# Kernel tuning notes

Measured on AMD Instinct MI355X. Metric: run time of the kernel, lower is better.

## Reference

```python
import jax, jax.numpy as jnp
import numpy as np

N_NODES = 50000
N_EDGES = 1600000
N_GRAPHS = 64
F_IN = 256
H = 1024
EPS = 1e-5


def setup_inputs() -> dict:
    key = jax.random.key(0)
    ks = jax.random.split(key, 6)
    x = jax.random.normal(ks[0], (N_NODES, F_IN), dtype=jnp.float32)
    edge_index = jax.random.randint(ks[1], (2, N_EDGES), 0, N_NODES, dtype=jnp.int32)
    batch = jnp.sort(jax.random.randint(ks[2], (N_NODES,), 0, N_GRAPHS, dtype=jnp.int32))
    # Glorot-ish init for GCN weights
    W0 = jax.random.normal(ks[3], (F_IN, H), dtype=jnp.float32) * (1.0 / np.sqrt(F_IN))
    b0 = jnp.zeros((H,), dtype=jnp.float32)
    Ws = jax.random.normal(ks[4], (3, H, H), dtype=jnp.float32) * (1.0 / np.sqrt(H))
    bs = jnp.zeros((3, H), dtype=jnp.float32)
    gammas = jnp.ones((4, H), dtype=jnp.float32)
    betas = jnp.zeros((4, H), dtype=jnp.float32)
    return {"x": x, "edge_index": edge_index, "batch": batch,
            "W0": W0, "b0": b0, "Ws": Ws, "bs": bs,
            "gammas": gammas, "betas": betas}


def _gcn_norm(edge_index, n_nodes):
    # Add self-loops (PyG GCNConv default), compute symmetric normalization.
    loops = jnp.arange(n_nodes, dtype=edge_index.dtype)
    row = jnp.concatenate([edge_index[0], loops])  # sources
    col = jnp.concatenate([edge_index[1], loops])  # targets (aggregation index)
    ones = jnp.ones(row.shape[0], dtype=jnp.float32)
    deg = jax.ops.segment_sum(ones, col, num_segments=n_nodes)
    dinv = jnp.where(deg > 0, jax.lax.rsqrt(deg), 0.0)
    norm = dinv[row] * dinv[col]  # [E + N]
    return row, col, norm


def _layer(h, W, b, gamma, beta, row, col, norm):
    ht = h @ W                                           # [N, H] GEMM
    msg = ht[row] * norm[:, None]                        # gather + scale
    agg = jax.ops.segment_sum(msg, col, num_segments=N_NODES) + b
    mu = jnp.mean(agg, axis=-1, keepdims=True)
    var = jnp.mean(jnp.square(agg - mu), axis=-1, keepdims=True)
    hn = (agg - mu) * jax.lax.rsqrt(var + EPS) * gamma + beta
    return jax.nn.relu(hn)


def reference(x, edge_index, batch, W0, b0, Ws, bs, gammas, betas):
    row, col, norm = _gcn_norm(edge_index, N_NODES)
    h = _layer(x, W0, b0, gammas[0], betas[0], row, col, norm)
    for i in range(3):
        h = _layer(h, Ws[i], bs[i], gammas[i + 1], betas[i + 1], row, col, norm)
    # scatter_mean over batch (graph-level pooling)
    sums = jax.ops.segment_sum(h, batch, num_segments=N_GRAPHS)
    cnt = jax.ops.segment_sum(jnp.ones((N_NODES,), jnp.float32), batch, num_segments=N_GRAPHS)
    return sums / jnp.maximum(cnt, 1.0)[:, None]
```

## Files before the change

kernel.cpp:

```cpp
#include <hip/hip_runtime.h>
#include <hip/hip_bf16.h>
#include <stdint.h>

#define NN 50000
#define NE 1600000
#define NG 64
#define FIN 256
#define HD 1024
#define EPSV 1e-5f

typedef __bf16 bf16;
typedef float f32x4 __attribute__((ext_vector_type(4)));
typedef int i32x4 __attribute__((ext_vector_type(4)));

typedef const __attribute__((address_space(1))) void* gptr_as1;
typedef __attribute__((address_space(3))) void* lptr_as3;

__device__ __forceinline__ void load_g2l_16(const void* g, const void* l) {
  __builtin_amdgcn_global_load_lds((gptr_as1)(uintptr_t)g,
                                   (lptr_as3)(uint32_t)(uintptr_t)l, 16, 0, 0);
}

__global__ void hist_kernel(const int* __restrict__ col, int* __restrict__ cnt, int E) {
  int e = blockIdx.x * 256 + threadIdx.x;
  if (e < E) atomicAdd(&cnt[col[e]], 1);
}

__global__ void dinv_kernel(const int* __restrict__ cnt, float* __restrict__ dinv, int n) {
  int i = blockIdx.x * 256 + threadIdx.x;
  if (i < n) dinv[i] = rsqrtf((float)(cnt[i] + 1));
}

__global__ void scan_partial_kernel(const int* __restrict__ cnt, int* __restrict__ partial, int n) {
  __shared__ int red[4];
  int i = blockIdx.x * 256 + threadIdx.x;
  int v = (i < n) ? cnt[i] : 0;
  #pragma unroll
  for (int off = 32; off; off >>= 1) v += __shfl_down(v, off, 64);
  if ((threadIdx.x & 63) == 0) red[threadIdx.x >> 6] = v;
  __syncthreads();
  if (threadIdx.x == 0) partial[blockIdx.x] = red[0] + red[1] + red[2] + red[3];
}

__global__ void scan_scan_kernel(int* __restrict__ partial, int nb) {
  __shared__ int s[256];
  int t = threadIdx.x;
  int v = (t < nb) ? partial[t] : 0;
  s[t] = v;
  __syncthreads();
  for (int off = 1; off < 256; off <<= 1) {
    int x = (t >= off) ? s[t - off] : 0;
    __syncthreads();
    s[t] += x;
    __syncthreads();
  }
  if (t < nb) partial[t] = s[t] - v;
}

__global__ void scan_final_kernel(const int* __restrict__ cnt, const int* __restrict__ partial,
                                  int* __restrict__ row_ptr, int n, int E) {
  __shared__ int s[256];
  int t = threadIdx.x;
  int i = blockIdx.x * 256 + t;
  int v = (i < n) ? cnt[i] : 0;
  s[t] = v;
  __syncthreads();
  for (int off = 1; off < 256; off <<= 1) {
    int x = (t >= off) ? s[t - off] : 0;
    __syncthreads();
    s[t] += x;
    __syncthreads();
  }
  if (i < n) row_ptr[i] = partial[blockIdx.x] + s[t] - v;
  if (i == 0) row_ptr[n] = E;
}

__global__ void scatter_kernel(const int* __restrict__ rowi, const int* __restrict__ coli,
                               const int* __restrict__ row_ptr, int* __restrict__ fill,
                               const float* __restrict__ dinv,
                               int* __restrict__ csr_src, float* __restrict__ csr_w, int E) {
  int e = blockIdx.x * 256 + threadIdx.x;
  if (e >= E) return;
  int s = rowi[e], d = coli[e];
  int pos = row_ptr[d] + atomicAdd(&fill[d], 1);
  csr_src[pos] = s;
  csr_w[pos] = dinv[s] * dinv[d];
}

__global__ __launch_bounds__(256) void quant_x_kernel(const float* __restrict__ x,
                                                      int8_t* __restrict__ A8,
                                                      float* __restrict__ hscale) {
  int row = blockIdx.x * 4 + (threadIdx.x >> 6);
  int t = threadIdx.x & 63;
  float4 v = ((const float4*)(x + (size_t)row * FIN))[t];
  float m = fmaxf(fmaxf(fabsf(v.x), fabsf(v.y)), fmaxf(fabsf(v.z), fabsf(v.w)));
  #pragma unroll
  for (int off = 32; off; off >>= 1) m = fmaxf(m, __shfl_xor(m, off, 64));
  float inv = (m > 0.f) ? 127.0f / m : 0.f;
  int q0 = min(127, max(-127, __float2int_rn(v.x * inv)));
  int q1 = min(127, max(-127, __float2int_rn(v.y * inv)));
  int q2 = min(127, max(-127, __float2int_rn(v.z * inv)));
  int q3 = min(127, max(-127, __float2int_rn(v.w * inv)));
  uint32_t p = ((uint32_t)(q0 & 0xff)) | ((uint32_t)(q1 & 0xff) << 8) |
               ((uint32_t)(q2 & 0xff) << 16) | ((uint32_t)(q3 & 0xff) << 24);
  ((uint32_t*)A8)[(size_t)row * 64 + t] = p;
  if (t == 0) hscale[row] = (m > 0.f) ? m / 127.0f : 0.f;
}

__global__ void wamax_kernel(const float* __restrict__ W, uint32_t* __restrict__ colmax,
                             int K, int N) {
  __shared__ float lds[8][32];
  int n = blockIdx.x * 32 + threadIdx.x;
  int k0 = blockIdx.y * 128;
  int kend = min(k0 + 128, K);
  float m = 0.f;
  for (int k = k0 + threadIdx.y; k < kend; k += 8)
    m = fmaxf(m, fabsf(W[(size_t)k * N + n]));
  lds[threadIdx.y][threadIdx.x] = m;
  __syncthreads();
  if (threadIdx.y == 0) {
    #pragma unroll
    for (int i = 1; i < 8; i++) m = fmaxf(m, lds[i][threadIdx.x]);
    atomicMax(&colmax[n], __float_as_uint(m));
  }
}

__global__ void wscale_kernel(const uint32_t* __restrict__ colmax, float* __restrict__ wscale) {
  int n = blockIdx.x * 256 + threadIdx.x;
  if (n < HD) {
    float m = __uint_as_float(colmax[n]);
    wscale[n] = (m > 0.f) ? m / 127.0f : 0.f;
  }
}

__global__ void transpose_wq8_kernel(const float* __restrict__ W,
                                     const uint32_t* __restrict__ colmax,
                                     int8_t* __restrict__ Wt8, int K, int N) {
  __shared__ float tile[32][33];
  int n0 = blockIdx.x * 32, k0 = blockIdx.y * 32;
  int tx = threadIdx.x, ty = threadIdx.y;
  #pragma unroll
  for (int i = ty; i < 32; i += 8) tile[i][tx] = W[(size_t)(k0 + i) * N + n0 + tx];
  __syncthreads();
  #pragma unroll
  for (int i = ty; i < 32; i += 8) {
    float cm = __uint_as_float(colmax[n0 + i]);
    float inv = (cm > 0.f) ? 127.0f / cm : 0.f;
    int q = min(127, max(-127, __float2int_rn(tile[tx][i] * inv)));
    Wt8[(size_t)(n0 + i) * K + k0 + tx] = (int8_t)q;
  }
}

__global__ __launch_bounds__(256, 2) void gemm_i8_q8_kernel(
    const int8_t* __restrict__ A8, const float* __restrict__ hscale,
    const int8_t* __restrict__ Wt8, const float* __restrict__ wscale,
    uint8_t* __restrict__ C8, float* __restrict__ scales, int M, int K) {
  __shared__ __align__(16) int8_t As[2][128 * 64];
  __shared__ __align__(16) int8_t Bs[2][128 * 64];
  __shared__ float smax[2][128];
  const int tid = threadIdx.x;
  const int w = tid >> 6, l = tid & 63;

  const int nwg = gridDim.x;
  const int o = blockIdx.x;
  const int lid = (o & 7) * (nwg >> 3) + (o >> 3);
  const int m0 = (lid >> 3) * 128, n0 = (lid & 7) * 128;
  const int cb = lid & 7;
  const int wr = w >> 1, wc = w & 1;

  i32x4 acc[4][4] = {};

  const int r0 = tid >> 2;
  const int c16 = (tid & 3) * 16;
  int ar0 = m0 + r0;       if (ar0 >= M) ar0 = M - 1;
  int ar1 = m0 + r0 + 64;  if (ar1 >= M) ar1 = M - 1;
  const int8_t* a0 = A8 + (size_t)ar0 * K + c16;
  const int8_t* a1 = A8 + (size_t)ar1 * K + c16;
  const int8_t* b0 = Wt8 + (size_t)(n0 + r0) * K + c16;
  const int8_t* b1 = Wt8 + (size_t)(n0 + r0 + 64) * K + c16;

  const int mrow = l & 15;
  const int kch = (l >> 4) * 16;

  auto stage = [&](int b, int k) {
    int8_t* asw = &As[b][w * 1024];
    int8_t* bsw = &Bs[b][w * 1024];
    load_g2l_16(a0 + k, asw);
    load_g2l_16(a1 + k, asw + 4096);
    load_g2l_16(b0 + k, bsw);
    load_g2l_16(b1 + k, bsw + 4096);
  };

  const int nit = K >> 6;
  stage(0, 0);
  __syncthreads();

  int cur = 0;
  for (int t = 0; t < nit; ++t) {
    if (t + 1 < nit) stage(cur ^ 1, (t + 1) << 6);
    i32x4 af[4], bf_[4];
    #pragma unroll
    for (int m = 0; m < 4; m++)
      af[m] = *(const i32x4*)&As[cur][(wr * 64 + m * 16 + mrow) * 64 + kch];
    #pragma unroll
    for (int n = 0; n < 4; n++)
      bf_[n] = *(const i32x4*)&Bs[cur][(wc * 64 + n * 16 + mrow) * 64 + kch];
    #pragma unroll
    for (int m = 0; m < 4; m++)
      #pragma unroll
      for (int n = 0; n < 4; n++)
        acc[m][n] = __builtin_amdgcn_mfma_i32_16x16x64_i8(af[m], bf_[n], acc[m][n], 0, 0, 0);
    __syncthreads();
    cur ^= 1;
  }

  float wsv[4];
  #pragma unroll
  for (int n = 0; n < 4; n++) wsv[n] = wscale[n0 + wc * 64 + n * 16 + (l & 15)];

  float cf[4][4][4];
  #pragma unroll
  for (int m = 0; m < 4; m++) {
    #pragma unroll
    for (int r = 0; r < 4; r++) {
      int rl = wr * 64 + m * 16 + (l >> 4) * 4 + r;
      int grow = m0 + rl; if (grow >= M) grow = M - 1;
      float hs = hscale[grow];
      float v = 0.f;
      #pragma unroll
      for (int n = 0; n < 4; n++) {
        float c = (float)acc[m][n][r] * hs * wsv[n];
        cf[m][n][r] = c;
        v = fmaxf(v, fabsf(c));
      }
      #pragma unroll
      for (int mask = 1; mask < 16; mask <<= 1) v = fmaxf(v, __shfl_xor(v, mask, 64));
      if ((l & 15) == 0) smax[wc][rl] = v;
    }
  }
  __syncthreads();

  #pragma unroll
  for (int m = 0; m < 4; m++) {
    #pragma unroll
    for (int r = 0; r < 4; r++) {
      int rl = wr * 64 + m * 16 + (l >> 4) * 4 + r;
      int grow = m0 + rl;
      float mx = fmaxf(smax[0][rl], smax[1][rl]);
      float inv = (mx > 0.f) ? 127.0f / mx : 0.f;
      if (grow < M) {
        if (wc == 0 && (l & 15) == 0)
          scales[(size_t)grow * 8 + cb] = (mx > 0.f) ? mx / 127.0f : 0.f;
        #pragma unroll
        for (int n = 0; n < 4; n++) {
          int gcol = n0 + wc * 64 + n * 16 + (l & 15);
          int u = __float2int_rn(cf[m][n][r] * inv) + 128;
          C8[(size_t)grow * HD + gcol] = (uint8_t)u;
        }
      }
    }
  }
}

__device__ __forceinline__ void acc_u8(float acc[8], float& sw, float w, uint2 d) {
  sw += w;
  acc[0] += w * (float)(d.x & 0xffu);
  acc[1] += w * (float)((d.x >> 8) & 0xffu);
  acc[2] += w * (float)((d.x >> 16) & 0xffu);
  acc[3] += w * (float)(d.x >> 24);
  acc[4] += w * (float)(d.y & 0xffu);
  acc[5] += w * (float)((d.y >> 8) & 0xffu);
  acc[6] += w * (float)((d.y >> 16) & 0xffu);
  acc[7] += w * (float)(d.y >> 24);
}

__global__ __launch_bounds__(256) void agg_ln_u8_kernel(
    const uint8_t* __restrict__ htu8, const float* __restrict__ scales,
    const int* __restrict__ row_ptr,
    const int* __restrict__ csr_src, const float* __restrict__ csr_w,
    const float* __restrict__ dinv, const float* __restrict__ bias,
    const float* __restrict__ gamma, const float* __restrict__ beta,
    int8_t* __restrict__ hq, float* __restrict__ hscale) {
  const int g = threadIdx.x >> 7;
  const int node = blockIdx.x * 2 + g;
  const int tt = threadIdx.x & 127;
  const int cbL = tt >> 4;
  const int wid = threadIdx.x >> 6;
  __shared__ float red[4];

  float acc[8] = {};
  float sw = 0.f;

  float dn = dinv[node];
  float wself = dn * dn * scales[(size_t)node * 8 + cbL];
  acc_u8(acc, sw, wself, ((const uint2*)(htu8 + (size_t)node * HD))[tt]);

  int e = row_ptr[node];
  const int e1 = row_ptr[node + 1];
  for (; e + 4 <= e1; e += 4) {
    int s0 = csr_src[e], s1 = csr_src[e + 1], s2 = csr_src[e + 2], s3 = csr_src[e + 3];
    float w0 = csr_w[e] * scales[(size_t)s0 * 8 + cbL];
    float w1 = csr_w[e + 1] * scales[(size_t)s1 * 8 + cbL];
    float w2 = csr_w[e + 2] * scales[(size_t)s2 * 8 + cbL];
    float w3 = csr_w[e + 3] * scales[(size_t)s3 * 8 + cbL];
    uint2 d0 = ((const uint2*)(htu8 + (size_t)s0 * HD))[tt];
    uint2 d1 = ((const uint2*)(htu8 + (size_t)s1 * HD))[tt];
    uint2 d2 = ((const uint2*)(htu8 + (size_t)s2 * HD))[tt];
    uint2 d3 = ((const uint2*)(htu8 + (size_t)s3 * HD))[tt];
    acc_u8(acc, sw, w0, d0);
    acc_u8(acc, sw, w1, d1);
    acc_u8(acc, sw, w2, d2);
    acc_u8(acc, sw, w3, d3);
  }
  for (; e < e1; e++) {
    int src = csr_src[e];
    float wgt = csr_w[e] * scales[(size_t)src * 8 + cbL];
    acc_u8(acc, sw, wgt, ((const uint2*)(htu8 + (size_t)src * HD))[tt]);
  }

  const float4* bias2 = (const float4*)bias;
  float4 ba = bias2[tt * 2], bb = bias2[tt * 2 + 1];
  float c128 = 128.0f * sw;
  acc[0] += ba.x - c128; acc[1] += ba.y - c128; acc[2] += ba.z - c128; acc[3] += ba.w - c128;
  acc[4] += bb.x - c128; acc[5] += bb.y - c128; acc[6] += bb.z - c128; acc[7] += bb.w - c128;

  float s = 0.f;
  #pragma unroll
  for (int j = 0; j < 8; j++) s += acc[j];
  #pragma unroll
  for (int off = 32; off; off >>= 1) s += __shfl_down(s, off, 64);
  if ((threadIdx.x & 63) == 0) red[wid] = s;
  __syncthreads();
  float mean = (red[g * 2] + red[g * 2 + 1]) * (1.0f / HD);
  __syncthreads();

  float d[8], s2 = 0.f;
  #pragma unroll
  for (int j = 0; j < 8; j++) { d[j] = acc[j] - mean; s2 += d[j] * d[j]; }
  #pragma unroll
  for (int off = 32; off; off >>= 1) s2 += __shfl_down(s2, off, 64);
  if ((threadIdx.x & 63) == 0) red[wid] = s2;
  __syncthreads();
  float var = (red[g * 2] + red[g * 2 + 1]) * (1.0f / HD);
  float rstd = rsqrtf(var + EPSV);

  const float4* gam2 = (const float4*)gamma;
  const float4* bet2 = (const float4*)beta;
  float4 g0 = gam2[tt * 2], g1 = gam2[tt * 2 + 1];
  float4 be0 = bet2[tt * 2], be1 = bet2[tt * 2 + 1];
  float gv[8] = {g0.x, g0.y, g0.z, g0.w, g1.x, g1.y, g1.z, g1.w};
  float bv[8] = {be0.x, be0.y, be0.z, be0.w, be1.x, be1.y, be1.z, be1.w};
  float o[8];
  float rmax = 0.f;
  #pragma unroll
  for (int j = 0; j < 8; j++) {
    o[j] = fmaxf(d[j] * rstd * gv[j] + bv[j], 0.0f);
    rmax = fmaxf(rmax, o[j]);
  }

  __syncthreads();
  #pragma unroll
  for (int off = 32; off; off >>= 1) rmax = fmaxf(rmax, __shfl_xor(rmax, off, 64));
  if ((threadIdx.x & 63) == 0) red[wid] = rmax;
  __syncthreads();
  float rm = fmaxf(red[g * 2], red[g * 2 + 1]);
  float qinv = (rm > 0.f) ? 127.0f / rm : 0.f;
  int q[8];
  #pragma unroll
  for (int j = 0; j < 8; j++) q[j] = min(127, __float2int_rn(o[j] * qinv));
  uint32_t p0 = ((uint32_t)q[0]) | ((uint32_t)q[1] << 8) | ((uint32_t)q[2] << 16) | ((uint32_t)q[3] << 24);
  uint32_t p1 = ((uint32_t)q[4]) | ((uint32_t)q[5] << 8) | ((uint32_t)q[6] << 16) | ((uint32_t)q[7] << 24);
  uint2 pk; pk.x = p0; pk.y = p1;
  ((uint2*)(hq + (size_t)node * HD))[tt] = pk;
  if (tt == 0) hscale[node] = (rm > 0.f) ? rm / 127.0f : 0.f;
}

__global__ void starts_kernel(const int* __restrict__ batch, int* __restrict__ start,
                              int n, int ngraph) {
  int g = blockIdx.x * blockDim.x + threadIdx.x;
  if (g > ngraph) return;
  int lo = 0, hi = n;
  while (lo < hi) {
    int mid = (lo + hi) >> 1;
    if (batch[mid] < g) lo = mid + 1; else hi = mid;
  }
  start[g] = lo;
}

#define POOL_CHUNKS 8
__global__ void pool_partial_kernel(const int8_t* __restrict__ hq,
                                    const float* __restrict__ hscale,
                                    const int* __restrict__ start,
                                    float* __restrict__ out) {
  int g = blockIdx.y, c = blockIdx.x;
  int t = threadIdx.x;
  int s0 = start[g], s1 = start[g + 1];
  int len = s1 - s0;
  int per = (len + POOL_CHUNKS - 1) / POOL_CHUNKS;
  int a = s0 + c * per;
  int b = min(a + per, s1);
  if (a >= b) return;
  f32x4 acc = {0.f, 0.f, 0.f, 0.f};
  for (int n = a; n < b; n++) {
    float hs = hscale[n];
    uint32_t d = ((const uint32_t*)(hq + (size_t)n * HD))[t];
    acc[0] += hs * (float)(d & 0xffu);
    acc[1] += hs * (float)((d >> 8) & 0xffu);
    acc[2] += hs * (float)((d >> 16) & 0xffu);
    acc[3] += hs * (float)(d >> 24);
  }
  float* o = out + (size_t)g * HD + t * 4;
  atomicAdd(o + 0, acc[0]);
  atomicAdd(o + 1, acc[1]);
  atomicAdd(o + 2, acc[2]);
  atomicAdd(o + 3, acc[3]);
}

__global__ void pool_div_kernel(float* __restrict__ out, const int* __restrict__ start) {
  int i = blockIdx.x * 256 + threadIdx.x;
  if (i >= NG * HD) return;
  int g = i >> 10;
  float c = (float)max(start[g + 1] - start[g], 1);
  out[i] = out[i] / c;
}

extern "C" void kernel_launch(void* const* d_in, const int* in_sizes, int n_in,
                              void* d_out, int out_size, void* d_ws, size_t ws_size,
                              hipStream_t stream) {
  const float* x      = (const float*)d_in[0];
  const int*   eidx   = (const int*)d_in[1];
  const int*   batch  = (const int*)d_in[2];
  const float* W0     = (const float*)d_in[3];
  const float* b0     = (const float*)d_in[4];
  const float* Ws     = (const float*)d_in[5];
  const float* bs     = (const float*)d_in[6];
  const float* gammas = (const float*)d_in[7];
  const float* betas  = (const float*)d_in[8];
  float* out = (float*)d_out;

  const int* erow = eidx;
  const int* ecol = eidx + NE;

  char* ws = (char*)d_ws;
  size_t off = 0;
  auto alloc = [&](size_t bytes) {
    void* p = ws + off;
    off = (off + bytes + 255) & ~(size_t)255;
    return p;
  };
  int*     cnt     = (int*)alloc((size_t)NN * 4);
  int*     row_ptr = (int*)alloc((size_t)(NN + 1) * 4);
  int*     fill    = (int*)alloc((size_t)NN * 4);
  int*     partial = (int*)alloc(256 * 4);
  float*   dinv    = (float*)alloc((size_t)NN * 4);
  int*     csr_src = (int*)alloc((size_t)NE * 4);
  float*   csr_w   = (float*)alloc((size_t)NE * 4);
  int8_t*  Wt8     = (int8_t*)alloc((size_t)HD * HD);
  int8_t*  A8      = (int8_t*)alloc((size_t)NN * HD);
  uint8_t* ht8     = (uint8_t*)alloc((size_t)NN * HD);
  float*   scales  = (float*)alloc((size_t)NN * 8 * 4);
  int*     gstart  = (int*)alloc(65 * 4);

  float*    wscale = (float*)cnt;
  uint32_t* colmax = (uint32_t*)cnt + 1024;
  float*    hscale = (float*)fill;

  hipMemsetAsync(cnt, 0, (size_t)NN * 4, stream);
  hipMemsetAsync(fill, 0, (size_t)NN * 4, stream);
  hipMemsetAsync(out, 0, (size_t)NG * HD * 4, stream);

  hist_kernel<<<(NE + 255) / 256, 256, 0, stream>>>(ecol, cnt, NE);
  dinv_kernel<<<(NN + 255) / 256, 256, 0, stream>>>(cnt, dinv, NN);
  int nb = (NN + 255) / 256;
  scan_partial_kernel<<<nb, 256, 0, stream>>>(cnt, partial, NN);
  scan_scan_kernel<<<1, 256, 0, stream>>>(partial, nb);
  scan_final_kernel<<<nb, 256, 0, stream>>>(cnt, partial, row_ptr, NN, NE);
  scatter_kernel<<<(NE + 255) / 256, 256, 0, stream>>>(erow, ecol, row_ptr, fill, dinv,
                                                       csr_src, csr_w, NE);
  starts_kernel<<<1, 128, 0, stream>>>(batch, gstart, NN, NG);

  quant_x_kernel<<<NN / 4, 256, 0, stream>>>(x, A8, hscale);

  const int nmt = (NN + 127) / 128;
  for (int L = 0; L < 4; L++) {
    int K = (L == 0) ? FIN : HD;
    const float* W    = (L == 0) ? W0 : Ws + (size_t)(L - 1) * HD * HD;
    const float* bias = (L == 0) ? b0 : bs + (size_t)(L - 1) * HD;
    hipMemsetAsync(colmax, 0, HD * 4, stream);
    wamax_kernel<<<dim3(HD / 32, (K + 127) / 128), dim3(32, 8), 0, stream>>>(W, colmax, K, HD);
    wscale_kernel<<<HD / 256, 256, 0, stream>>>(colmax, wscale);
    transpose_wq8_kernel<<<dim3(HD / 32, K / 32), dim3(32, 8), 0, stream>>>(W, colmax, Wt8, K, HD);
    gemm_i8_q8_kernel<<<nmt * 8, 256, 0, stream>>>(A8, hscale, Wt8, wscale, ht8, scales, NN, K);
    agg_ln_u8_kernel<<<NN / 2, 256, 0, stream>>>(ht8, scales, row_ptr, csr_src, csr_w,
                                                 dinv, bias, gammas + (size_t)L * HD,
                                                 betas + (size_t)L * HD, A8, hscale);
  }

  pool_partial_kernel<<<dim3(POOL_CHUNKS, NG), 256, 0, stream>>>(A8, hscale, gstart, out);
  pool_div_kernel<<<(NG * HD + 255) / 256, 256, 0, stream>>>(out, gstart);
}
```

Before: 1.581 ms.

## Batch weight quantization, pack CSR edges, raise GEMM occupancy, pack aggregation FMAs

Quantizes and transposes all four layer weights in one set of launches before the layer loop, which removes 16 small launches and memsets from the critical path. Stores each CSR edge's source index and weight together as an int2, so every edge needs one load instead of two. Moves the GEMM to launch_bounds(256,4) and drops the cf register array by recomputing the dequantized value in the store pass, to cut register pressure and raise occupancy. Uses f32x2 vector accumulators in aggregation so the compiler can emit packed FMAs. The risk is spills at the tighter register bound and slightly different float rounding order in the GEMM epilogue.

```diff
diff --git a/kernel.cpp b/kernel.cpp
--- a/kernel.cpp
+++ b/kernel.cpp
@@ -11,6 +11,7 @@
 
 typedef __bf16 bf16;
 typedef float f32x4 __attribute__((ext_vector_type(4)));
+typedef float f32x2 __attribute__((ext_vector_type(2)));
 typedef int i32x4 __attribute__((ext_vector_type(4)));
 
 typedef const __attribute__((address_space(1))) void* gptr_as1;
@@ -78,13 +79,15 @@
 __global__ void scatter_kernel(const int* __restrict__ rowi, const int* __restrict__ coli,
                                const int* __restrict__ row_ptr, int* __restrict__ fill,
                                const float* __restrict__ dinv,
-                               int* __restrict__ csr_src, float* __restrict__ csr_w, int E) {
+                               int2* __restrict__ csr_sw, int E) {
   int e = blockIdx.x * 256 + threadIdx.x;
   if (e >= E) return;
   int s = rowi[e], d = coli[e];
   int pos = row_ptr[d] + atomicAdd(&fill[d], 1);
-  csr_src[pos] = s;
-  csr_w[pos] = dinv[s] * dinv[d];
+  int2 p;
+  p.x = s;
+  p.y = __float_as_int(dinv[s] * dinv[d]);
+  csr_sw[pos] = p;
 }
 
 __global__ __launch_bounds__(256) void quant_x_kernel(const float* __restrict__ x,
@@ -107,51 +110,67 @@
   if (t == 0) hscale[row] = (m > 0.f) ? m / 127.0f : 0.f;
 }
 
-__global__ void wamax_kernel(const float* __restrict__ W, uint32_t* __restrict__ colmax,
-                             int K, int N) {
+__device__ __forceinline__ const float* layer_W(const float* W0, const float* Ws, int L) {
+  return (L == 0) ? W0 : Ws + (size_t)(L - 1) * HD * HD;
+}
+
+__global__ void wamax_all_kernel(const float* __restrict__ W0, const float* __restrict__ Ws,
+                                 uint32_t* __restrict__ colmax) {
   __shared__ float lds[8][32];
+  int L = blockIdx.z;
+  int K = (L == 0) ? FIN : HD;
+  int k0 = blockIdx.y * 128;
+  if (k0 >= K) return;
+  const float* W = layer_W(W0, Ws, L);
   int n = blockIdx.x * 32 + threadIdx.x;
-  int k0 = blockIdx.y * 128;
   int kend = min(k0 + 128, K);
   float m = 0.f;
   for (int k = k0 + threadIdx.y; k < kend; k += 8)
-    m = fmaxf(m, fabsf(W[(size_t)k * N + n]));
+    m = fmaxf(m, fabsf(W[(size_t)k * HD + n]));
   lds[threadIdx.y][threadIdx.x] = m;
   __syncthreads();
   if (threadIdx.y == 0) {
     #pragma unroll
     for (int i = 1; i < 8; i++) m = fmaxf(m, lds[i][threadIdx.x]);
-    atomicMax(&colmax[n], __float_as_uint(m));
-  }
-}
-
-__global__ void wscale_kernel(const uint32_t* __restrict__ colmax, float* __restrict__ wscale) {
-  int n = blockIdx.x * 256 + threadIdx.x;
-  if (n < HD) {
-    float m = __uint_as_float(colmax[n]);
-    wscale[n] = (m > 0.f) ? m / 127.0f : 0.f;
-  }
-}
-
-__global__ void transpose_wq8_kernel(const float* __restrict__ W,
-                                     const uint32_t* __restrict__ colmax,
-                                     int8_t* __restrict__ Wt8, int K, int N) {
+    atomicMax(&colmax[L * HD + n], __float_as_uint(m));
+  }
+}
+
+__global__ void wscale_all_kernel(const uint32_t* __restrict__ colmax,
+                                  float* __restrict__ wscale) {
+  int i = blockIdx.x * 256 + threadIdx.x;
+  if (i < 4 * HD) {
+    float m = __uint_as_float(colmax[i]);
+    wscale[i] = (m > 0.f) ? m / 127.0f : 0.f;
+  }
+}
+
+__global__ void transpose_wq8_all_kernel(const float* __restrict__ W0,
+                                         const float* __restrict__ Ws,
+                                         const uint32_t* __restrict__ colmax,
+                                         int8_t* __restrict__ Wt8_all) {
   __shared__ float tile[32][33];
-  int n0 = blockIdx.x * 32, k0 = blockIdx.y * 32;
+  int L = blockIdx.z;
+  int K = (L == 0) ? FIN : HD;
+  int k0 = blockIdx.y * 32;
+  if (k0 >= K) return;
+  const float* W = layer_W(W0, Ws, L);
+  int8_t* Wt8 = Wt8_all + ((L == 0) ? 0 : (size_t)FIN * HD + (size_t)(L - 1) * HD * HD);
+  int n0 = blockIdx.x * 32;
   int tx = threadIdx.x, ty = threadIdx.y;
   #pragma unroll
-  for (int i = ty; i < 32; i += 8) tile[i][tx] = W[(size_t)(k0 + i) * N + n0 + tx];
+  for (int i = ty; i < 32; i += 8) tile[i][tx] = W[(size_t)(k0 + i) * HD + n0 + tx];
   __syncthreads();
   #pragma unroll
   for (int i = ty; i < 32; i += 8) {
-    float cm = __uint_as_float(colmax[n0 + i]);
+    float cm = __uint_as_float(colmax[L * HD + n0 + i]);
     float inv = (cm > 0.f) ? 127.0f / cm : 0.f;
     int q = min(127, max(-127, __float2int_rn(tile[tx][i] * inv)));
     Wt8[(size_t)(n0 + i) * K + k0 + tx] = (int8_t)q;
   }
 }
 
-__global__ __launch_bounds__(256, 2) void gemm_i8_q8_kernel(
+__global__ __launch_bounds__(256, 4) void gemm_i8_q8_kernel(
     const int8_t* __restrict__ A8, const float* __restrict__ hscale,
     const int8_t* __restrict__ Wt8, const float* __restrict__ wscale,
     uint8_t* __restrict__ C8, float* __restrict__ scales, int M, int K) {
@@ -218,21 +237,17 @@
   #pragma unroll
   for (int n = 0; n < 4; n++) wsv[n] = wscale[n0 + wc * 64 + n * 16 + (l & 15)];
 
-  float cf[4][4][4];
   #pragma unroll
   for (int m = 0; m < 4; m++) {
     #pragma unroll
     for (int r = 0; r < 4; r++) {
       int rl = wr * 64 + m * 16 + (l >> 4) * 4 + r;
       int grow = m0 + rl; if (grow >= M) grow = M - 1;
-      float hs = hscale[grow];
       float v = 0.f;
       #pragma unroll
-      for (int n = 0; n < 4; n++) {
-        float c = (float)acc[m][n][r] * hs * wsv[n];
-        cf[m][n][r] = c;
-        v = fmaxf(v, fabsf(c));
-      }
+      for (int n = 0; n < 4; n++)
+        v = fmaxf(v, fabsf((float)acc[m][n][r] * wsv[n]));
+      v *= hscale[grow];
       #pragma unroll
       for (int mask = 1; mask < 16; mask <<= 1) v = fmaxf(v, __shfl_xor(v, mask, 64));
       if ((l & 15) == 0) smax[wc][rl] = v;
@@ -249,12 +264,13 @@
       float mx = fmaxf(smax[0][rl], smax[1][rl]);
       float inv = (mx > 0.f) ? 127.0f / mx : 0.f;
       if (grow < M) {
+        float hs = hscale[grow];
         if (wc == 0 && (l & 15) == 0)
           scales[(size_t)grow * 8 + cb] = (mx > 0.f) ? mx / 127.0f : 0.f;
         #pragma unroll
         for (int n = 0; n < 4; n++) {
           int gcol = n0 + wc * 64 + n * 16 + (l & 15);
-          int u = __float2int_rn(cf[m][n][r] * inv) + 128;
+          int u = __float2int_rn((float)acc[m][n][r] * hs * wsv[n] * inv) + 128;
           C8[(size_t)grow * HD + gcol] = (uint8_t)u;
         }
       }
@@ -262,22 +278,22 @@
   }
 }
 
-__device__ __forceinline__ void acc_u8(float acc[8], float& sw, float w, uint2 d) {
+__device__ __forceinline__ void acc_u8p(f32x2 a[4], float& sw, float w, uint2 d) {
   sw += w;
-  acc[0] += w * (float)(d.x & 0xffu);
-  acc[1] += w * (float)((d.x >> 8) & 0xffu);
-  acc[2] += w * (float)((d.x >> 16) & 0xffu);
-  acc[3] += w * (float)(d.x >> 24);
-  acc[4] += w * (float)(d.y & 0xffu);
-  acc[5] += w * (float)((d.y >> 8) & 0xffu);
-  acc[6] += w * (float)((d.y >> 16) & 0xffu);
-  acc[7] += w * (float)(d.y >> 24);
+  f32x2 w2 = {w, w};
+  f32x2 v0 = {(float)(d.x & 0xffu), (float)((d.x >> 8) & 0xffu)};
+  f32x2 v1 = {(float)((d.x >> 16) & 0xffu), (float)(d.x >> 24)};
+  f32x2 v2 = {(float)(d.y & 0xffu), (float)((d.y >> 8) & 0xffu)};
+  f32x2 v3 = {(float)((d.y >> 16) & 0xffu), (float)(d.y >> 24)};
+  a[0] += w2 * v0;
+  a[1] += w2 * v1;
+  a[2] += w2 * v2;
+  a[3] += w2 * v3;
 }
 
 __global__ __launch_bounds__(256) void agg_ln_u8_kernel(
     const uint8_t* __restrict__ htu8, const float* __restrict__ scales,
-    const int* __restrict__ row_ptr,
-    const int* __restrict__ csr_src, const float* __restrict__ csr_w,
+    const int* __restrict__ row_ptr, const int2* __restrict__ csr_sw,
     const float* __restrict__ dinv, const float* __restrict__ bias,
     const float* __restrict__ gamma, const float* __restrict__ beta,
     int8_t* __restrict__ hq, float* __restrict__ hscale) {
@@ -288,35 +304,38 @@
   const int wid = threadIdx.x >> 6;
   __shared__ float red[4];
 
-  float acc[8] = {};
+  f32x2 acc2[4] = {};
   float sw = 0.f;
 
   float dn = dinv[node];
   float wself = dn * dn * scales[(size_t)node * 8 + cbL];
-  acc_u8(acc, sw, wself, ((const uint2*)(htu8 + (size_t)node * HD))[tt]);
+  acc_u8p(acc2, sw, wself, ((const uint2*)(htu8 + (size_t)node * HD))[tt]);
 
   int e = row_ptr[node];
   const int e1 = row_ptr[node + 1];
   for (; e + 4 <= e1; e += 4) {
-    int s0 = csr_src[e], s1 = csr_src[e + 1], s2 = csr_src[e + 2], s3 = csr_src[e + 3];
-    float w0 = csr_w[e] * scales[(size_t)s0 * 8 + cbL];
-    float w1 = csr_w[e + 1] * scales[(size_t)s1 * 8 + cbL];
-    float w2 = csr_w[e + 2] * scales[(size_t)s2 * 8 + cbL];
-    float w3 = csr_w[e + 3] * scales[(size_t)s3 * 8 + cbL];
-    uint2 d0 = ((const uint2*)(htu8 + (size_t)s0 * HD))[tt];
-    uint2 d1 = ((const uint2*)(htu8 + (size_t)s1 * HD))[tt];
-    uint2 d2 = ((const uint2*)(htu8 + (size_t)s2 * HD))[tt];
-    uint2 d3 = ((const uint2*)(htu8 + (size_t)s3 * HD))[tt];
-    acc_u8(acc, sw, w0, d0);
-    acc_u8(acc, sw, w1, d1);
-    acc_u8(acc, sw, w2, d2);
-    acc_u8(acc, sw, w3, d3);
+    int2 p0 = csr_sw[e], p1 = csr_sw[e + 1], p2 = csr_sw[e + 2], p3 = csr_sw[e + 3];
+    float w0 = __int_as_float(p0.y) * scales[(size_t)p0.x * 8 + cbL];
+    float w1 = __int_as_float(p1.y) * scales[(size_t)p1.x * 8 + cbL];
+    float w2 = __int_as_float(p2.y) * scales[(size_t)p2.x * 8 + cbL];
+    float w3 = __int_as_float(p3.y) * scales[(size_t)p3.x * 8 + cbL];
+    uint2 d0 = ((const uint2*)(htu8 + (size_t)p0.x * HD))[tt];
+    uint2 d1 = ((const uint2*)(htu8 + (size_t)p1.x * HD))[tt];
+    uint2 d2 = ((const uint2*)(htu8 + (size_t)p2.x * HD))[tt];
+    uint2 d3 = ((const uint2*)(htu8 + (size_t)p3.x * HD))[tt];
+    acc_u8p(acc2, sw, w0, d0);
+    acc_u8p(acc2, sw, w1, d1);
+    acc_u8p(acc2, sw, w2, d2);
+    acc_u8p(acc2, sw, w3, d3);
   }
   for (; e < e1; e++) {
-    int src = csr_src[e];
-    float wgt = csr_w[e] * scales[(size_t)src * 8 + cbL];
-    acc_u8(acc, sw, wgt, ((const uint2*)(htu8 + (size_t)src * HD))[tt]);
-  }
+    int2 p = csr_sw[e];
+    float wgt = __int_as_float(p.y) * scales[(size_t)p.x * 8 + cbL];
+    acc_u8p(acc2, sw, wgt, ((const uint2*)(htu8 + (size_t)p.x * HD))[tt]);
+  }
+
+  float acc[8] = {acc2[0][0], acc2[0][1], acc2[1][0], acc2[1][1],
+                  acc2[2][0], acc2[2][1], acc2[3][0], acc2[3][1]};
 
   const float4* bias2 = (const float4*)bias;
   float4 ba = bias2[tt * 2], bb = bias2[tt * 2 + 1];
@@ -453,16 +472,15 @@
   int*     fill    = (int*)alloc((size_t)NN * 4);
   int*     partial = (int*)alloc(256 * 4);
   float*   dinv    = (float*)alloc((size_t)NN * 4);
-  int*     csr_src = (int*)alloc((size_t)NE * 4);
-  float*   csr_w   = (float*)alloc((size_t)NE * 4);
-  int8_t*  Wt8     = (int8_t*)alloc((size_t)HD * HD);
+  int2*    csr_sw  = (int2*)alloc((size_t)NE * 8);
+  int8_t*  Wt8     = (int8_t*)alloc((size_t)FIN * HD + 3 * (size_t)HD * HD);
   int8_t*  A8      = (int8_t*)alloc((size_t)NN * HD);
   uint8_t* ht8     = (uint8_t*)alloc((size_t)NN * HD);
   float*   scales  = (float*)alloc((size_t)NN * 8 * 4);
   int*     gstart  = (int*)alloc(65 * 4);
 
   float*    wscale = (float*)cnt;
-  uint32_t* colmax = (uint32_t*)cnt + 1024;
+  uint32_t* colmax = (uint32_t*)cnt + 4096;
   float*    hscale = (float*)fill;
 
   hipMemsetAsync(cnt, 0, (size_t)NN * 4, stream);
@@ -476,22 +494,25 @@
   scan_scan_kernel<<<1, 256, 0, stream>>>(partial, nb);
   scan_final_kernel<<<nb, 256, 0, stream>>>(cnt, partial, row_ptr, NN, NE);
   scatter_kernel<<<(NE + 255) / 256, 256, 0, stream>>>(erow, ecol, row_ptr, fill, dinv,
-                                                       csr_src, csr_w, NE);
+                                                       csr_sw, NE);
   starts_kernel<<<1, 128, 0, stream>>>(batch, gstart, NN, NG);
 
   quant_x_kernel<<<NN / 4, 256, 0, stream>>>(x, A8, hscale);
+
+  hipMemsetAsync(colmax, 0, 4 * HD * 4, stream);
+  wamax_all_kernel<<<dim3(HD / 32, 8, 4), dim3(32, 8), 0, stream>>>(W0, Ws, colmax);
+  wscale_all_kernel<<<(4 * HD) / 256, 256, 0, stream>>>(colmax, wscale);
+  transpose_wq8_all_kernel<<<dim3(HD / 32, HD / 32, 4), dim3(32, 8), 0, stream>>>(
+      W0, Ws, colmax, Wt8);
 
   const int nmt = (NN + 127) / 128;
   for (int L = 0; L < 4; L++) {
     int K = (L == 0) ? FIN : HD;
-    const float* W    = (L == 0) ? W0 : Ws + (size_t)(L - 1) * HD * HD;
+    const int8_t* WtL = Wt8 + ((L == 0) ? 0 : (size_t)FIN * HD + (size_t)(L - 1) * HD * HD);
     const float* bias = (L == 0) ? b0 : bs + (size_t)(L - 1) * HD;
-    hipMemsetAsync(colmax, 0, HD * 4, stream);
-    wamax_kernel<<<dim3(HD / 32, (K + 127) / 128), dim3(32, 8), 0, stream>>>(W, colmax, K, HD);
-    wscale_kernel<<<HD / 256, 256, 0, stream>>>(colmax, wscale);
-    transpose_wq8_kernel<<<dim3(HD / 32, K / 32), dim3(32, 8), 0, stream>>>(W, colmax, Wt8, K, HD);
-    gemm_i8_q8_kernel<<<nmt * 8, 256, 0, stream>>>(A8, hscale, Wt8, wscale, ht8, scales, NN, K);
-    agg_ln_u8_kernel<<<NN / 2, 256, 0, stream>>>(ht8, scales, row_ptr, csr_src, csr_w,
+    gemm_i8_q8_kernel<<<nmt * 8, 256, 0, stream>>>(A8, hscale, WtL, wscale + L * HD,
+                                                   ht8, scales, NN, K);
+    agg_ln_u8_kernel<<<NN / 2, 256, 0, stream>>>(ht8, scales, row_ptr, csr_sw,
                                                  dinv, bias, gammas + (size_t)L * HD,
                                                  betas + (size_t)L * HD, A8, hscale);
   }
```

Result: faster. 1.544 ms (-2.3%).
